# Optimization experiments

Measured on AMD Instinct MI355X. Metric: run time of the kernel, lower is better.

The kernel has to match this reference:

```python
import jax, jax.numpy as jnp
import numpy as np

B, S, D = 2, 2048, 2048
H, KVH, HD = 16, 4, 128
GROUPS = H // KVH
SCALE = HD ** -0.5


def rotate_half(x):
    half = x.shape[-1] // 2
    return jnp.concatenate((-x[..., half:], x[..., :half]), axis=-1)


def apply_rope(q, k, cos, sin):
    # q,k: [B,S,H,HD]; cos,sin: [S,HD//2] -> repeat_interleave(2) -> [S,HD]
    cos = jnp.repeat(cos, 2, axis=-1)[None, :, None, :]
    sin = jnp.repeat(sin, 2, axis=-1)[None, :, None, :]
    return q * cos + rotate_half(q) * sin, k * cos + rotate_half(k) * sin


def setup_inputs() -> dict:
    key = jax.random.key(0)
    ks = jax.random.split(key, 8)
    inp = {
        'x': jax.random.normal(ks[0], (B, S, D), dtype=jnp.float32),
        'cos': jnp.cos(jnp.arange(S, dtype=jnp.float32)[:, None] * (1.0 / (10000.0 ** (jnp.arange(HD // 2, dtype=jnp.float32) / (HD // 2))))[None, :].reshape(1, HD // 2)),
        'sin': None,
        'mask': jnp.tril(jnp.ones((S, S), dtype=bool))[None, None, :, :],
        'Wq': jax.random.normal(ks[1], (D, H * HD), dtype=jnp.float32) * (D ** -0.5),
        'Wk': jax.random.normal(ks[2], (D, KVH * HD), dtype=jnp.float32) * (D ** -0.5),
        'Wv': jax.random.normal(ks[3], (D, KVH * HD), dtype=jnp.float32) * (D ** -0.5),
        'Wo': jax.random.normal(ks[4], (H * HD, D), dtype=jnp.float32) * ((H * HD) ** -0.5),
    }
    inv_freq = 1.0 / (10000.0 ** (jnp.arange(0, HD // 2, dtype=jnp.float32) / (HD // 2)))
    freqs = jnp.arange(S, dtype=jnp.float32)[:, None] * inv_freq[None, :]  # [S, HD//2]
    inp['cos'] = jnp.cos(freqs)
    inp['sin'] = jnp.sin(freqs)
    return inp


def reference(x, cos, sin, mask, Wq, Wk, Wv, Wo):
    b, s, _ = x.shape
    q = (x @ Wq).reshape(b, s, H, HD)    # [B,S,H,HD]
    k = (x @ Wk).reshape(b, s, KVH, HD)  # [B,S,KVH,HD]
    v = (x @ Wv).reshape(b, s, KVH, HD)
    q, k = apply_rope(q, k, cos, sin)
    q = q.transpose(0, 2, 1, 3)  # [B,H,S,HD]
    k = k.transpose(0, 2, 1, 3)  # [B,KVH,S,HD]
    v = v.transpose(0, 2, 1, 3)
    k = jnp.repeat(k, GROUPS, axis=1)  # [B,H,S,HD]
    v = jnp.repeat(v, GROUPS, axis=1)
    scores = jnp.einsum('bhqd,bhkd->bhqk', q, k) * SCALE
    scores = jnp.where(mask, scores, -jnp.inf)
    attn = jax.nn.softmax(scores, axis=-1)
    out = jnp.einsum('bhqk,bhkd->bhqd', attn, v)
    out = out.transpose(0, 2, 1, 3).reshape(b, s, H * HD)
    return out @ Wo
```

## Files before the change

kernel.cpp:

```cpp
#include <hip/hip_runtime.h>
#include <hip/hip_bf16.h>
#include <cstdint>
#include <type_traits>

typedef __attribute__((ext_vector_type(8))) short short8;
typedef __attribute__((ext_vector_type(4))) float floatx4;

constexpr int S_LEN = 2048;
constexpr float ATTN_SCALE = 0.08838834764831845f;
constexpr float LOG2E = 1.4426950408889634f;
constexpr float CP = ATTN_SCALE * LOG2E;
constexpr float THRR = 5.0f / CP;

__device__ __forceinline__ void gl_lds16(const void* gp, void* lp) {
  __builtin_amdgcn_global_load_lds(
      (__attribute__((address_space(1))) void*)(uintptr_t)gp,
      (__attribute__((address_space(3))) void*)lp,
      16, 0, 0);
}

__device__ __forceinline__ void rope8(short8 x0, short8 x1, const float* ca,
                                      const float* sa, const float* cb,
                                      const float* sb, short8& y0, short8& y1) {
#pragma unroll
  for (int e = 0; e < 8; ++e) {
    union { short s; __hip_bfloat16 h; } u0, u1, w0, w1;
    u0.s = x0[e]; u1.s = x1[e];
    float f0 = __bfloat162float(u0.h), f1 = __bfloat162float(u1.h);
    int j = e >> 1;
    w0.h = __float2bfloat16(f0 * ca[j] - f1 * sa[j]);
    w1.h = __float2bfloat16(f1 * cb[j] + f0 * sb[j]);
    y0[e] = w0.s; y1[e] = w1.s;
  }
}

__device__ __forceinline__ void tr32(const float* __restrict__ src,
                                     __hip_bfloat16* __restrict__ dst,
                                     int blk, int nblk_x, int N, int tid,
                                     float (*tile)[33]) {
  int n0 = (blk % nblk_x) * 32, k0 = (blk / nblk_x) * 32;
  int tx = tid & 31, ty = tid >> 5;
#pragma unroll
  for (int i = ty; i < 32; i += 8)
    tile[i][tx] = src[(size_t)(k0 + i) * N + n0 + tx];
  __syncthreads();
#pragma unroll
  for (int i = ty; i < 32; i += 8)
    dst[(size_t)(n0 + i) * 2048 + k0 + tx] = __float2bfloat16(tile[tx][i]);
}

__global__ void prep_kernel(const float* __restrict__ x,
                            const float* __restrict__ Wq,
                            const float* __restrict__ Wk,
                            const float* __restrict__ Wv,
                            const float* __restrict__ Wo,
                            __hip_bfloat16* __restrict__ xb,
                            __hip_bfloat16* __restrict__ wqkvt,
                            __hip_bfloat16* __restrict__ wot) {
  __shared__ float tile[32][33];
  int bx = blockIdx.x, tid = threadIdx.x;
  if (bx < 8192) {
    int i = bx * 256 + tid;
    float4 f = reinterpret_cast<const float4*>(x)[i];
    union { unsigned long long u64; __hip_bfloat16 h[4]; } u;
    u.h[0] = __float2bfloat16(f.x);
    u.h[1] = __float2bfloat16(f.y);
    u.h[2] = __float2bfloat16(f.z);
    u.h[3] = __float2bfloat16(f.w);
    reinterpret_cast<unsigned long long*>(xb)[i] = u.u64;
  } else if (bx < 12288) {
    tr32(Wq, wqkvt, bx - 8192, 64, 2048, tid, tile);
  } else if (bx < 13312) {
    tr32(Wk, wqkvt + 2048 * 2048, bx - 12288, 16, 512, tid, tile);
  } else if (bx < 14336) {
    tr32(Wv, wqkvt + 2560 * 2048, bx - 13312, 16, 512, tid, tile);
  } else {
    tr32(Wo, wot, bx - 14336, 64, 2048, tid, tile);
  }
}

__device__ __forceinline__ void gemm256_core(
    const __hip_bfloat16* __restrict__ Ab,
    const __hip_bfloat16* __restrict__ Bb,
    const int K, __hip_bfloat16* lds, floatx4 (&acc)[8][4]) {
  const int tid = threadIdx.x;
  const int wave = tid >> 6, lane = tid & 63;
  const int quad = lane >> 4, l15 = lane & 15;
  const int wm = wave >> 2, wn = wave & 3;
  const int nt = K >> 6;
  const int u2 = wave * 2;

  auto stA = [&](int tt, int h) {
    __hip_bfloat16* dst = lds + (tt & 1) * 32768;
    const int k0 = tt << 6;
#pragma unroll
    for (int j = 0; j < 2; ++j) {
      const int kc = (u2 + j) >> 1, rb = (u2 + j) & 1;
      gl_lds16(Ab + (size_t)(h * 128 + rb * 64 + lane) * K + k0 + kc * 8,
               dst + (kc * 256 + h * 128 + rb * 64) * 8);
    }
  };
  auto stB = [&](int tt, int h) {
    __hip_bfloat16* dst = lds + (tt & 1) * 32768 + 16384;
    const int k0 = tt << 6;
#pragma unroll
    for (int j = 0; j < 2; ++j) {
      const int kc = (u2 + j) >> 1, rb = (u2 + j) & 1;
      gl_lds16(Bb + (size_t)(h * 128 + rb * 64 + lane) * K + k0 + kc * 8,
               dst + (kc * 256 + h * 128 + rb * 64) * 8);
    }
  };

  stA(0, 0); stA(0, 1); stB(0, 0); stB(0, 1);
  if (nt > 1) { stB(1, 0); stB(1, 1); }
  asm volatile("s_waitcnt vmcnt(4)" ::: "memory");
  __builtin_amdgcn_s_barrier();

  const int abase = (quad * 256 + wm * 128 + l15) * 8;
  const int bbase = (quad * 256 + wn * 64 + l15) * 8;

#pragma unroll 2
  for (int t = 0; t < nt; ++t) {
    const __hip_bfloat16* Al = lds + (t & 1) * 32768;
    const __hip_bfloat16* Bl = Al + 16384;
    short8 b[2][4];
#pragma unroll
    for (int q = 0; q < 4; ++q) {
      short8 a[2][2];
#pragma unroll
      for (int kk = 0; kk < 2; ++kk) {
        if (q == 0) {
#pragma unroll
          for (int ni = 0; ni < 4; ++ni)
            b[kk][ni] = *(const short8*)&Bl[kk * 8192 + bbase + ni * 128];
        }
#pragma unroll
        for (int mi = 0; mi < 2; ++mi)
          a[kk][mi] = *(const short8*)&Al[kk * 8192 + abase + (2 * q + mi) * 128];
      }
      if (q == 0)      { if (t + 1 < nt) stA(t + 1, 0); }
      else if (q == 1) { if (t + 1 < nt) stA(t + 1, 1); }
      else if (q == 2) { if (t + 2 < nt) stB(t + 2, 0); }
      else             { if (t + 2 < nt) stB(t + 2, 1); }
      __builtin_amdgcn_s_barrier();
      asm volatile("s_waitcnt lgkmcnt(0)" ::: "memory");
      __builtin_amdgcn_sched_barrier(0);
      __builtin_amdgcn_s_setprio(1);
#pragma unroll
      for (int kk = 0; kk < 2; ++kk)
#pragma unroll
        for (int mi = 0; mi < 2; ++mi)
#pragma unroll
          for (int ni = 0; ni < 4; ++ni)
            acc[2 * q + mi][ni] = __builtin_amdgcn_mfma_f32_16x16x32_bf16(
                a[kk][mi], b[kk][ni], acc[2 * q + mi][ni], 0, 0, 0);
      __builtin_amdgcn_s_setprio(0);
      if (q == 3) {
        if (t + 2 < nt) asm volatile("s_waitcnt vmcnt(4)" ::: "memory");
        else            asm volatile("s_waitcnt vmcnt(0)" ::: "memory");
      }
      __builtin_amdgcn_s_barrier();
    }
  }
  asm volatile("" ::: "memory");
}

__device__ __forceinline__ void gemm_256x128_core(
    const __hip_bfloat16* __restrict__ Ab,
    const __hip_bfloat16* __restrict__ Bb,
    const int K, __hip_bfloat16* lds, floatx4 (&acc)[4][4]) {
  const int tid = threadIdx.x;
  const int wave = tid >> 6, lane = tid & 63;
  const int quad = lane >> 4, l15 = lane & 15;
  const int wm = wave >> 1, wn = wave & 1;
  const int nt = K >> 6;

  auto stA = [&](int tt, int c) {
    __hip_bfloat16* dst = lds + (tt & 1) * 24576;
    const int k0 = tt << 6;
    const int i = c * 8 + wave;
    const int kc = i >> 2, rb = i & 3;
    gl_lds16(Ab + (size_t)(rb * 64 + lane) * K + k0 + kc * 8,
             dst + (kc * 256 + rb * 64) * 8);
  };
  auto stB = [&](int tt, int c) {
    __hip_bfloat16* dst = lds + (tt & 1) * 24576 + 16384;
    const int k0 = tt << 6;
    const int i = c * 8 + wave;
    const int kc = i >> 1, rb = i & 1;
    gl_lds16(Bb + (size_t)(rb * 64 + lane) * K + k0 + kc * 8,
             dst + (kc * 128 + rb * 64) * 8);
  };

  stA(0, 0); stA(0, 1); stA(0, 2); stA(0, 3);
  stB(0, 0); stB(0, 1);
  if (nt > 1) {
    stB(1, 0); stB(1, 1);
    asm volatile("s_waitcnt vmcnt(2)" ::: "memory");
  } else {
    asm volatile("s_waitcnt vmcnt(0)" ::: "memory");
  }
  __builtin_amdgcn_s_barrier();

  const int abase = (quad * 256 + wm * 64 + l15) * 8;
  const int bbase = (quad * 128 + wn * 64 + l15) * 8;

#pragma unroll 2
  for (int t = 0; t < nt; ++t) {
    const __hip_bfloat16* Al = lds + (t & 1) * 24576;
    const __hip_bfloat16* Bl = Al + 16384;
    short8 b[2][4], a[2][2];
#pragma unroll
    for (int kk = 0; kk < 2; ++kk) {
#pragma unroll
      for (int ni = 0; ni < 4; ++ni)
        b[kk][ni] = *(const short8*)&Bl[kk * 4096 + bbase + ni * 128];
#pragma unroll
      for (int mi = 0; mi < 2; ++mi)
        a[kk][mi] = *(const short8*)&Al[kk * 8192 + abase + mi * 128];
    }
    if (t + 1 < nt) { stA(t + 1, 0); stA(t + 1, 1); }
    __builtin_amdgcn_s_barrier();
    asm volatile("s_waitcnt lgkmcnt(0)" ::: "memory");
    __builtin_amdgcn_sched_barrier(0);
    __builtin_amdgcn_s_setprio(1);
#pragma unroll
    for (int kk = 0; kk < 2; ++kk)
#pragma unroll
      for (int mi = 0; mi < 2; ++mi)
#pragma unroll
        for (int ni = 0; ni < 4; ++ni)
          acc[mi][ni] = __builtin_amdgcn_mfma_f32_16x16x32_bf16(
              a[kk][mi], b[kk][ni], acc[mi][ni], 0, 0, 0);
    __builtin_amdgcn_s_setprio(0);
    __builtin_amdgcn_s_barrier();
#pragma unroll
    for (int kk = 0; kk < 2; ++kk)
#pragma unroll
      for (int mi = 0; mi < 2; ++mi)
        a[kk][mi] = *(const short8*)&Al[kk * 8192 + abase + (2 + mi) * 128];
    if (t + 1 < nt) { stA(t + 1, 2); stA(t + 1, 3); }
    if (t + 2 < nt) { stB(t + 2, 0); stB(t + 2, 1); }
    __builtin_amdgcn_s_barrier();
    asm volatile("s_waitcnt lgkmcnt(0)" ::: "memory");
    __builtin_amdgcn_sched_barrier(0);
    __builtin_amdgcn_s_setprio(1);
#pragma unroll
    for (int kk = 0; kk < 2; ++kk)
#pragma unroll
      for (int mi = 0; mi < 2; ++mi)
#pragma unroll
        for (int ni = 0; ni < 4; ++ni)
          acc[2 + mi][ni] = __builtin_amdgcn_mfma_f32_16x16x32_bf16(
              a[kk][mi], b[kk][ni], acc[2 + mi][ni], 0, 0, 0);
    __builtin_amdgcn_s_setprio(0);
    if (t + 2 < nt) asm volatile("s_waitcnt vmcnt(2)" ::: "memory");
    else            asm volatile("s_waitcnt vmcnt(0)" ::: "memory");
    __builtin_amdgcn_s_barrier();
  }
  asm volatile("" ::: "memory");
}

__global__ __launch_bounds__(512, 2) void qkv_gemm_kernel(
    const __hip_bfloat16* __restrict__ A,
    const __hip_bfloat16* __restrict__ Bt,
    __hip_bfloat16* __restrict__ qbuf,
    __hip_bfloat16* __restrict__ kbuf,
    __hip_bfloat16* __restrict__ vbuf,
    const float* __restrict__ cosb,
    const float* __restrict__ sinb) {
  constexpr int K = 2048;
  __shared__ __align__(16) __hip_bfloat16 lds[65536];
  const int tid = threadIdx.x;
  const int m0 = blockIdx.y * 256, n0 = blockIdx.x * 256;

  floatx4 acc[8][4] = {};
  gemm256_core(A + (size_t)m0 * K, Bt + (size_t)n0 * K, K, lds, acc);

  const int wave = tid >> 6, lane = tid & 63;
  const int quad = lane >> 4, l15 = lane & 15;
  const int wm = wave >> 2, wn = wave & 3;
  const bool isv = (n0 >= 2560);
  short* lds2 = (short*)lds;
#pragma unroll
  for (int mi = 0; mi < 8; ++mi)
#pragma unroll
    for (int ni = 0; ni < 4; ++ni)
#pragma unroll
      for (int r = 0; r < 4; ++r) {
        int row = wm * 128 + mi * 16 + quad * 4 + r;
        int col = wn * 64 + ni * 16 + l15;
        union { short s; __hip_bfloat16 h; } u;
        u.h = __float2bfloat16(acc[mi][ni][r]);
        if (isv) lds2[col * 256 + row] = u.s;
        else     lds2[row * 256 + col] = u.s;
      }
  __syncthreads();

  const int c16 = tid & 15, hh = c16 >> 3, c8 = c16 & 7;
  const int rid = tid >> 4, d0 = c8 * 8;
  if (n0 < 2048) {
#pragma unroll
    for (int j = 0; j < 8; ++j) {
      int rr = rid + 32 * j;
      int rowg = m0 + rr;
      int s = rowg & (S_LEN - 1);
      float ca[4], sa[4], cb[4], sb[4];
      *(float4*)ca = *(const float4*)&cosb[s * 64 + c8 * 4];
      *(float4*)sa = *(const float4*)&sinb[s * 64 + c8 * 4];
      *(float4*)cb = *(const float4*)&cosb[s * 64 + 32 + c8 * 4];
      *(float4*)sb = *(const float4*)&sinb[s * 64 + 32 + c8 * 4];
      short8 x0 = *(const short8*)&lds2[rr * 256 + hh * 128 + d0];
      short8 x1 = *(const short8*)&lds2[rr * 256 + hh * 128 + 64 + d0];
      short8 y0, y1;
      rope8(x0, x1, ca, sa, cb, sb, y0, y1);
      *(short8*)(qbuf + (size_t)rowg * 2048 + n0 + hh * 128 + d0) = y0;
      *(short8*)(qbuf + (size_t)rowg * 2048 + n0 + hh * 128 + 64 + d0) = y1;
    }
  } else if (!isv) {
    const int kvh = ((n0 - 2048) >> 7) + hh;
#pragma unroll
    for (int j = 0; j < 8; ++j) {
      int rr = rid + 32 * j;
      int rowg = m0 + rr;
      int s = rowg & (S_LEN - 1), bb = rowg >> 11;
      int kv = s & 63;
      size_t tb = ((size_t)(bb * 4 + kvh) * 32 + (s >> 6)) * 8192;
      float ca[4], sa[4], cb[4], sb[4];
      *(float4*)ca = *(const float4*)&cosb[s * 64 + c8 * 4];
      *(float4*)sa = *(const float4*)&sinb[s * 64 + c8 * 4];
      *(float4*)cb = *(const float4*)&cosb[s * 64 + 32 + c8 * 4];
      *(float4*)sb = *(const float4*)&sinb[s * 64 + 32 + c8 * 4];
      short8 x0 = *(const short8*)&lds2[rr * 256 + hh * 128 + d0];
      short8 x1 = *(const short8*)&lds2[rr * 256 + hh * 128 + 64 + d0];
      short8 y0, y1;
      rope8(x0, x1, ca, sa, cb, sb, y0, y1);
      *(short8*)(kbuf + tb + (size_t)c8 * 512 + kv * 8) = y0;
      *(short8*)(kbuf + tb + (size_t)(8 + c8) * 512 + kv * 8) = y1;
    }
  } else {
    const int kvh = ((n0 - 2560) >> 7) + hh;
    const int bb = m0 >> 11;
    const int kt0 = (m0 & (S_LEN - 1)) >> 6;
    const int kv0 = c8 * 8;
#pragma unroll
    for (int j = 0; j < 4; ++j) {
      int d = rid + 32 * j;
      int cxor = (d & 7) << 3;
#pragma unroll
      for (int half = 0; half < 4; ++half) {
        short8 vv = *(const short8*)&lds2[(hh * 128 + d) * 256 + half * 64 + kv0];
        size_t tb = ((size_t)(bb * 4 + kvh) * 32 + kt0 + half) * 8192;
        *(short8*)(vbuf + tb + d * 64 + (kv0 ^ cxor)) = vv;
      }
    }
  }
}

__global__ __launch_bounds__(512, 2) void gemm_bt_f32_kernel(
    const __hip_bfloat16* __restrict__ A,
    const __hip_bfloat16* __restrict__ Bt,
    float* __restrict__ C, int N, int K) {
  __shared__ __align__(16) __hip_bfloat16 lds[49152];
  const int tid = threadIdx.x;
  const int m0 = blockIdx.y * 256, n0 = blockIdx.x * 128;

  floatx4 acc[4][4] = {};
  gemm_256x128_core(A + (size_t)m0 * K, Bt + (size_t)n0 * K, K, lds, acc);

  const int wave = tid >> 6, lane = tid & 63;
  const int quad = lane >> 4, l15 = lane & 15;
  const int wm = wave >> 1, wn = wave & 1;
#pragma unroll
  for (int mi = 0; mi < 4; ++mi)
#pragma unroll
    for (int ni = 0; ni < 4; ++ni)
#pragma unroll
      for (int r = 0; r < 4; ++r) {
        int row = m0 + wm * 64 + mi * 16 + quad * 4 + r;
        int col = n0 + wn * 64 + ni * 16 + l15;
        C[(size_t)row * N + col] = acc[mi][ni][r];
      }
}

__global__ __launch_bounds__(256, 2) void attn_kernel(
    const __hip_bfloat16* __restrict__ qbuf,
    const __hip_bfloat16* __restrict__ kbuf,
    const __hip_bfloat16* __restrict__ vbuf,
    __hip_bfloat16* __restrict__ aout) {
  const int qt = blockIdx.x;
  const int bh = blockIdx.y;
  const int b = bh >> 4, h = bh & 15;
  const int kvh = h >> 2;

  __shared__ __align__(16) __hip_bfloat16 Kbuf[2][8192];
  __shared__ __align__(16) __hip_bfloat16 Vbuf[2][8192];

  const int tid = threadIdx.x;
  const int wave = tid >> 6, lane = tid & 63;
  const int quad = lane >> 4, l15 = lane & 15;

  short8 qfrag[2][4];
#pragma unroll
  for (int rs = 0; rs < 2; ++rs)
#pragma unroll
    for (int kc = 0; kc < 4; ++kc)
      qfrag[rs][kc] = *(const short8*)(qbuf +
          (size_t)(b * S_LEN + qt * 128 + rs * 64 + wave * 16 + l15) * 2048 +
          h * 128 + kc * 32 + quad * 8);

  const __hip_bfloat16* ktiles = kbuf + (size_t)(b * 4 + kvh) * 32 * 8192;
  const __hip_bfloat16* vtiles = vbuf + (size_t)(b * 4 + kvh) * 32 * 8192;
  const int nt = 2 * qt + 2;

#pragma unroll
  for (int j = 0; j < 4; ++j) {
    int c = tid + 256 * j;
    gl_lds16(ktiles + c * 8, &Kbuf[0][c * 8]);
    gl_lds16(vtiles + c * 8, &Vbuf[0][c * 8]);
  }

  float m_s[2] = {-1e30f, -1e30f};
  float l_s[2] = {0.f, 0.f};
  floatx4 o[2][8] = {};

  for (int kt = 0; kt < nt; ++kt) {
    const int cur = kt & 1;
    __syncthreads();

    if (kt + 1 < nt) {
      const __hip_bfloat16* kb = ktiles + (size_t)(kt + 1) * 8192;
      const __hip_bfloat16* vb = vtiles + (size_t)(kt + 1) * 8192;
#pragma unroll
      for (int j = 0; j < 4; ++j) {
        int c = tid + 256 * j;
        gl_lds16(kb + c * 8, &Kbuf[1 - cur][c * 8]);
        gl_lds16(vb + c * 8, &Vbuf[1 - cur][c * 8]);
      }
    }

    floatx4 sc[2][4] = {};
#pragma unroll
    for (int ni = 0; ni < 4; ++ni)
#pragma unroll
      for (int kc = 0; kc < 4; ++kc) {
        short8 bf = *(const short8*)&Kbuf[cur][((kc * 4 + quad) * 64 + ni * 16 + l15) * 8];
        sc[0][ni] = __builtin_amdgcn_mfma_f32_16x16x32_bf16(bf, qfrag[0][kc], sc[0][ni], 0, 0, 0);
        sc[1][ni] = __builtin_amdgcn_mfma_f32_16x16x32_bf16(bf, qfrag[1][kc], sc[1][ni], 0, 0, 0);
      }

    short8 pa[2][2];
#pragma unroll
    for (int rs = 0; rs < 2; ++rs) {
      const int qt64 = 2 * qt + rs;
      if (kt >= qt64) {
        const int qg = qt * 128 + rs * 64 + wave * 16 + l15;
#pragma unroll
        for (int ni = 0; ni < 4; ++ni) {
          int kvb = kt * 64 + ni * 16 + quad * 4;
#pragma unroll
          for (int r = 0; r < 4; ++r)
            if (kvb + r > qg) sc[rs][ni][r] = -1e30f;
        }
      }

      float v = sc[rs][0][0];
#pragma unroll
      for (int ni = 0; ni < 4; ++ni)
#pragma unroll
        for (int r = 0; r < 4; ++r) v = fmaxf(v, sc[rs][ni][r]);
      v = fmaxf(v, __shfl_xor(v, 16));
      v = fmaxf(v, __shfl_xor(v, 32));

      float mold = m_s[rs];
      if (__any(v > mold + THRR)) {
        float mnew = fmaxf(mold, v);
        float alpha = exp2f((mold - mnew) * CP);
        m_s[rs] = mnew;
        l_s[rs] *= alpha;
        float ar[4];
#pragma unroll
        for (int r = 0; r < 4; ++r)
          ar[r] = __shfl(alpha, (lane & 48) + quad * 4 + r);
#pragma unroll
        for (int nc = 0; nc < 8; ++nc)
#pragma unroll
          for (int r = 0; r < 4; ++r) o[rs][nc][r] *= ar[r];
      }

      float mc = m_s[rs] * CP;
      unsigned pk[4][2];
      float lsum = 0.f;
#pragma unroll
      for (int ni = 0; ni < 4; ++ni)
#pragma unroll
        for (int pr = 0; pr < 2; ++pr) {
          float p0 = exp2f(sc[rs][ni][2 * pr] * CP - mc);
          float p1 = exp2f(sc[rs][ni][2 * pr + 1] * CP - mc);
          lsum += p0 + p1;
          union { unsigned u; ushort us[2]; } uu;
          union { __hip_bfloat16 h; ushort us; } b0, b1;
          b0.h = __float2bfloat16(p0); b1.h = __float2bfloat16(p1);
          uu.us[0] = b0.us; uu.us[1] = b1.us;
          pk[ni][pr] = uu.u;
        }
      lsum += __shfl_xor(lsum, 16);
      lsum += __shfl_xor(lsum, 32);
      l_s[rs] += lsum;

#pragma unroll
      for (int kk2 = 0; kk2 < 2; ++kk2) {
        union { unsigned w[4]; short8 s; } pw_;
#pragma unroll
        for (int j = 0; j < 4; ++j) {
          int src = ((((quad & 1) * 2) + (j >> 1)) << 4) | l15;
          unsigned lo = (unsigned)__shfl((int)pk[2 * kk2][j & 1], src);
          unsigned hi = (unsigned)__shfl((int)pk[2 * kk2 + 1][j & 1], src);
          pw_.w[j] = (quad >> 1) ? hi : lo;
        }
        pa[rs][kk2] = pw_.s;
      }
    }

    __builtin_amdgcn_s_setprio(1);
#pragma unroll
    for (int kk2 = 0; kk2 < 2; ++kk2) {
#pragma unroll
      for (int nc = 0; nc < 8; ++nc) {
        int d = nc * 16 + l15;
        int swcol = (kk2 * 32 + quad * 8) ^ ((d & 7) << 3);
        short8 vv = *(const short8*)&Vbuf[cur][d * 64 + swcol];
        o[0][nc] = __builtin_amdgcn_mfma_f32_16x16x32_bf16(pa[0][kk2], vv, o[0][nc], 0, 0, 0);
        o[1][nc] = __builtin_amdgcn_mfma_f32_16x16x32_bf16(pa[1][kk2], vv, o[1][nc], 0, 0, 0);
      }
    }
    __builtin_amdgcn_s_setprio(0);
  }

#pragma unroll
  for (int rs = 0; rs < 2; ++rs) {
    float inv[4];
#pragma unroll
    for (int r = 0; r < 4; ++r) {
      float lr = __shfl(l_s[rs], (lane & 48) + quad * 4 + r);
      inv[r] = 1.0f / lr;
    }
    const size_t orow0 = (size_t)(b * S_LEN + qt * 128 + rs * 64 + wave * 16 + quad * 4);
#pragma unroll
    for (int nc = 0; nc < 8; ++nc)
#pragma unroll
      for (int r = 0; r < 4; ++r)
        aout[(orow0 + r) * 2048 + h * 128 + nc * 16 + l15] =
            __float2bfloat16(o[rs][nc][r] * inv[r]);
  }
}

extern "C" void kernel_launch(void* const* d_in, const int* in_sizes, int n_in,
                              void* d_out, int out_size, void* d_ws, size_t ws_size,
                              hipStream_t stream) {
  const float* x    = (const float*)d_in[0];
  const float* cosb = (const float*)d_in[1];
  const float* sinb = (const float*)d_in[2];
  const float* Wq = (const float*)d_in[4];
  const float* Wk = (const float*)d_in[5];
  const float* Wv = (const float*)d_in[6];
  const float* Wo = (const float*)d_in[7];
  float* out = (float*)d_out;

  char* ws = (char*)d_ws;
  __hip_bfloat16* xb    = (__hip_bfloat16*)(ws);
  __hip_bfloat16* wqkvt = (__hip_bfloat16*)(ws + (16u << 20));
  __hip_bfloat16* wot   = (__hip_bfloat16*)(ws + (28u << 20));
  __hip_bfloat16* qbuf  = (__hip_bfloat16*)(ws + (36u << 20));
  __hip_bfloat16* kbuf  = (__hip_bfloat16*)(ws + (52u << 20));
  __hip_bfloat16* vbuf  = (__hip_bfloat16*)(ws + (56u << 20));
  __hip_bfloat16* aout  = (__hip_bfloat16*)(ws + (60u << 20));

  prep_kernel<<<18432, 256, 0, stream>>>(x, Wq, Wk, Wv, Wo, xb, wqkvt, wot);
  qkv_gemm_kernel<<<dim3(12, 16), 512, 0, stream>>>(xb, wqkvt, qbuf, kbuf, vbuf, cosb, sinb);
  attn_kernel<<<dim3(16, 32), 256, 0, stream>>>(qbuf, kbuf, vbuf, aout);
  gemm_bt_f32_kernel<<<dim3(16, 16), 512, 0, stream>>>(aout, wot, out, 2048, 2048);
}
```

Before: 385.5 us.

## Pair causal query tiles j and 31-j per block to balance attention work

Each attention block now handles two 64-row query tiles, j and 31-j, instead of two adjacent tiles. The KV loop runs 32-j tiles, and the MFMAs, softmax and output for the near tile are skipped once it passes its causal diagonal. This evens out per-block work under the causal mask, which shortens the longest-running blocks and reduces tail imbalance. In exchange, blocks with a small j stream more K/V tiles, and the work skip adds a block-uniform branch inside the loop.

```diff
diff --git a/kernel.cpp b/kernel.cpp
--- a/kernel.cpp
+++ b/kernel.cpp
@@ -388,10 +388,11 @@
     const __hip_bfloat16* __restrict__ kbuf,
     const __hip_bfloat16* __restrict__ vbuf,
     __hip_bfloat16* __restrict__ aout) {
-  const int qt = blockIdx.x;
+  const int j = blockIdx.x;
   const int bh = blockIdx.y;
   const int b = bh >> 4, h = bh & 15;
   const int kvh = h >> 2;
+  const int jq[2] = {j, 31 - j};
 
   __shared__ __align__(16) __hip_bfloat16 Kbuf[2][8192];
   __shared__ __align__(16) __hip_bfloat16 Vbuf[2][8192];
@@ -406,16 +407,16 @@
 #pragma unroll
     for (int kc = 0; kc < 4; ++kc)
       qfrag[rs][kc] = *(const short8*)(qbuf +
-          (size_t)(b * S_LEN + qt * 128 + rs * 64 + wave * 16 + l15) * 2048 +
+          (size_t)(b * S_LEN + jq[rs] * 64 + wave * 16 + l15) * 2048 +
           h * 128 + kc * 32 + quad * 8);
 
   const __hip_bfloat16* ktiles = kbuf + (size_t)(b * 4 + kvh) * 32 * 8192;
   const __hip_bfloat16* vtiles = vbuf + (size_t)(b * 4 + kvh) * 32 * 8192;
-  const int nt = 2 * qt + 2;
-
-#pragma unroll
-  for (int j = 0; j < 4; ++j) {
-    int c = tid + 256 * j;
+  const int nt = 32 - j;
+
+#pragma unroll
+  for (int jj = 0; jj < 4; ++jj) {
+    int c = tid + 256 * jj;
     gl_lds16(ktiles + c * 8, &Kbuf[0][c * 8]);
     gl_lds16(vtiles + c * 8, &Vbuf[0][c * 8]);
   }
@@ -432,29 +433,32 @@
       const __hip_bfloat16* kb = ktiles + (size_t)(kt + 1) * 8192;
       const __hip_bfloat16* vb = vtiles + (size_t)(kt + 1) * 8192;
 #pragma unroll
-      for (int j = 0; j < 4; ++j) {
-        int c = tid + 256 * j;
+      for (int jj = 0; jj < 4; ++jj) {
+        int c = tid + 256 * jj;
         gl_lds16(kb + c * 8, &Kbuf[1 - cur][c * 8]);
         gl_lds16(vb + c * 8, &Vbuf[1 - cur][c * 8]);
       }
     }
 
+    const bool do0 = (kt <= j);
+
     floatx4 sc[2][4] = {};
 #pragma unroll
     for (int ni = 0; ni < 4; ++ni)
 #pragma unroll
       for (int kc = 0; kc < 4; ++kc) {
         short8 bf = *(const short8*)&Kbuf[cur][((kc * 4 + quad) * 64 + ni * 16 + l15) * 8];
-        sc[0][ni] = __builtin_amdgcn_mfma_f32_16x16x32_bf16(bf, qfrag[0][kc], sc[0][ni], 0, 0, 0);
+        if (do0)
+          sc[0][ni] = __builtin_amdgcn_mfma_f32_16x16x32_bf16(bf, qfrag[0][kc], sc[0][ni], 0, 0, 0);
         sc[1][ni] = __builtin_amdgcn_mfma_f32_16x16x32_bf16(bf, qfrag[1][kc], sc[1][ni], 0, 0, 0);
       }
 
     short8 pa[2][2];
 #pragma unroll
     for (int rs = 0; rs < 2; ++rs) {
-      const int qt64 = 2 * qt + rs;
-      if (kt >= qt64) {
-        const int qg = qt * 128 + rs * 64 + wave * 16 + l15;
+      if (rs == 0 && !do0) continue;
+      if (kt >= jq[rs]) {
+        const int qg = jq[rs] * 64 + wave * 16 + l15;
 #pragma unroll
         for (int ni = 0; ni < 4; ++ni) {
           int kvb = kt * 64 + ni * 16 + quad * 4;
@@ -512,11 +516,11 @@
       for (int kk2 = 0; kk2 < 2; ++kk2) {
         union { unsigned w[4]; short8 s; } pw_;
 #pragma unroll
-        for (int j = 0; j < 4; ++j) {
-          int src = ((((quad & 1) * 2) + (j >> 1)) << 4) | l15;
-          unsigned lo = (unsigned)__shfl((int)pk[2 * kk2][j & 1], src);
-          unsigned hi = (unsigned)__shfl((int)pk[2 * kk2 + 1][j & 1], src);
-          pw_.w[j] = (quad >> 1) ? hi : lo;
+        for (int jj = 0; jj < 4; ++jj) {
+          int src = ((((quad & 1) * 2) + (jj >> 1)) << 4) | l15;
+          unsigned lo = (unsigned)__shfl((int)pk[2 * kk2][jj & 1], src);
+          unsigned hi = (unsigned)__shfl((int)pk[2 * kk2 + 1][jj & 1], src);
+          pw_.w[jj] = (quad >> 1) ? hi : lo;
         }
         pa[rs][kk2] = pw_.s;
       }
@@ -530,7 +534,8 @@
         int d = nc * 16 + l15;
         int swcol = (kk2 * 32 + quad * 8) ^ ((d & 7) << 3);
         short8 vv = *(const short8*)&Vbuf[cur][d * 64 + swcol];
-        o[0][nc] = __builtin_amdgcn_mfma_f32_16x16x32_bf16(pa[0][kk2], vv, o[0][nc], 0, 0, 0);
+        if (do0)
+          o[0][nc] = __builtin_amdgcn_mfma_f32_16x16x32_bf16(pa[0][kk2], vv, o[0][nc], 0, 0, 0);
         o[1][nc] = __builtin_amdgcn_mfma_f32_16x16x32_bf16(pa[1][kk2], vv, o[1][nc], 0, 0, 0);
       }
     }
@@ -545,7 +550,7 @@
       float lr = __shfl(l_s[rs], (lane & 48) + quad * 4 + r);
       inv[r] = 1.0f / lr;
     }
-    const size_t orow0 = (size_t)(b * S_LEN + qt * 128 + rs * 64 + wave * 16 + quad * 4);
+    const size_t orow0 = (size_t)(b * S_LEN + jq[rs] * 64 + wave * 16 + quad * 4);
 #pragma unroll
     for (int nc = 0; nc < 8; ++nc)
 #pragma unroll
```

Result: faster. 359.2 us (-6.8%).
